# Performance work log

Measured on AMD Instinct MI355X. Metric: run time of the kernel, lower is better.

## Reference

```python
import jax, jax.numpy as jnp
import numpy as np

B, S, D, H = 4, 2048, 1024, 16
DK = D // H


def _rope(x):
    # x: [B, H, S, DK]; lucidrains rotary_embedding_torch default:
    # theta=10000, interleaved (rotate_half on (d/2, 2) pairs), freqs repeated pairwise.
    s, d = x.shape[-2], x.shape[-1]
    inv_freq = 1.0 / (10000.0 ** (jnp.arange(0, d, 2, dtype=jnp.float32) / d))  # [d/2]
    angles = jnp.arange(s, dtype=jnp.float32)[:, None] * inv_freq[None, :]      # [S, d/2]
    ang = jnp.repeat(angles, 2, axis=-1)                                        # [S, d] interleaved
    cos, sin = jnp.cos(ang), jnp.sin(ang)
    xp = x.reshape(*x.shape[:-1], d // 2, 2)
    rot = jnp.stack((-xp[..., 1], xp[..., 0]), axis=-1).reshape(x.shape)        # rotate_half
    return x * cos + rot * sin


def setup_inputs() -> dict:
    key = jax.random.key(0)
    ks = jax.random.split(key, 8)
    scale = 1.0 / np.sqrt(D)
    return {
        "q": jax.random.normal(ks[0], (B, S, D), dtype=jnp.float32),
        "k": jax.random.normal(ks[1], (B, S, D), dtype=jnp.float32),
        "v": jax.random.normal(ks[2], (B, S, D), dtype=jnp.float32),
        "mask": jax.random.randint(ks[3], (B, S), 0, 2, dtype=jnp.int32),
        "w_q": jax.random.normal(ks[4], (D, D), dtype=jnp.float32) * scale,
        "w_k": jax.random.normal(ks[5], (D, D), dtype=jnp.float32) * scale,
        "w_v": jax.random.normal(ks[6], (D, D), dtype=jnp.float32) * scale,
        "w_o": jax.random.normal(ks[7], (D, D), dtype=jnp.float32) * scale,
    }


def reference(q, k, v, mask, w_q, w_k, w_v, w_o):
    # Linear weights stored [out, in] as in torch; y = x @ W^T (bias=False).
    def split_heads(x):
        b, s, _ = x.shape
        return x.reshape(b, s, H, DK).transpose(0, 2, 1, 3)  # [B,H,S,DK]

    query = split_heads(q @ w_q.T)
    key_ = split_heads(k @ w_k.T)
    value = split_heads(v @ w_v.T)

    query = _rope(query)
    key_ = _rope(key_)

    scores = jnp.einsum("bhqd,bhkd->bhqk", query, key_) / np.sqrt(DK)
    scores = jnp.where(mask[:, None, None, :] == 0, -10000.0, scores)
    attn = jax.nn.softmax(scores, axis=-1)  # dropout is identity at eval
    x = jnp.einsum("bhqk,bhkd->bhqd", attn, value)
    x = x.transpose(0, 2, 1, 3).reshape(q.shape[0], -1, H * DK)
    return x @ w_o.T
```

## Files before the change

kernel.cpp:

```cpp
#include <hip/hip_runtime.h>
#include <hip/hip_bf16.h>
#include <math.h>


namespace {

constexpr int Bb = 4, Ss = 2048, Dd = 1024, Hh = 16, DKk = 64;

typedef __bf16 bf16;
typedef __attribute__((ext_vector_type(8))) __bf16 bf16x8;
typedef __attribute__((ext_vector_type(4))) float f32x4;

__device__ __forceinline__ bf16x8 pack8(float4 a, float4 b) {
  bf16x8 r;
  r[0] = (__bf16)a.x; r[1] = (__bf16)a.y; r[2] = (__bf16)a.z; r[3] = (__bf16)a.w;
  r[4] = (__bf16)b.x; r[5] = (__bf16)b.y; r[6] = (__bf16)b.z; r[7] = (__bf16)b.w;
  return r;
}

__device__ __forceinline__ void gl_lds16(const bf16* g, bf16* l) {
  __builtin_amdgcn_global_load_lds((const __attribute__((address_space(1))) void*)g,
                                   (__attribute__((address_space(3))) void*)l, 16, 0, 0);
}

__global__ __launch_bounds__(256) void cvt_pair(const float* __restrict__ x, bf16* __restrict__ xd,
                                                const float* __restrict__ ws, bf16* __restrict__ wd) {
  const int bid = blockIdx.x;
  const float* s; bf16* d; size_t idx;
  if (bid < 4096) { s = x; d = xd; idx = (size_t)bid * 256 + threadIdx.x; }
  else { s = ws; d = wd; idx = (size_t)(bid - 4096) * 256 + threadIdx.x; }
  idx *= 8;
  float4 f0 = *(const float4*)(s + idx), f1 = *(const float4*)(s + idx + 4);
  *(bf16x8*)(d + idx) = pack8(f0, f1);
}

__global__ __launch_bounds__(256) void cvt_w(const float* __restrict__ ws, bf16* __restrict__ wd) {
  size_t idx = ((size_t)blockIdx.x * 256 + threadIdx.x) * 8;
  float4 f0 = *(const float4*)(ws + idx), f1 = *(const float4*)(ws + idx + 4);
  *(bf16x8*)(wd + idx) = pack8(f0, f1);
}

template <int MODE>
__global__ __launch_bounds__(256) void mha_gemm(const bf16* __restrict__ A,
                                                const bf16* __restrict__ W,
                                                void* __restrict__ dstv) {
  __shared__ __align__(16) bf16 As[2][128][32];
  __shared__ __align__(16) bf16 Bs[2][128][32];
  const int tid = threadIdx.x;
  const int bm0 = blockIdx.x * 128, bn0 = blockIdx.y * 128;
  const int w = tid >> 6, lane = tid & 63, l16 = lane & 15, quad = lane >> 4;
  const int wm = (w >> 1) * 64, wn = (w & 1) * 64;
  const int lr = lane >> 2, lc = (lane & 3) * 8;

  const bf16* Ag = A + (size_t)(bm0 + w * 32 + lr) * Dd + lc;
  const bf16* Wg = W + (size_t)(bn0 + w * 32 + lr) * Dd + lc;

  f32x4 acc[4][4] = {};

  gl_lds16(Ag, &As[0][w * 32][0]);
  gl_lds16(Ag + 16 * Dd, &As[0][w * 32 + 16][0]);
  gl_lds16(Wg, &Bs[0][w * 32][0]);
  gl_lds16(Wg + 16 * Dd, &Bs[0][w * 32 + 16][0]);
  __syncthreads();

  for (int kt = 0; kt < 32; ++kt) {
    const int cur = kt & 1, nxt = cur ^ 1;
    if (kt < 31) {
      const int ko = (kt + 1) * 32;
      gl_lds16(Ag + ko, &As[nxt][w * 32][0]);
      gl_lds16(Ag + ko + 16 * Dd, &As[nxt][w * 32 + 16][0]);
      gl_lds16(Wg + ko, &Bs[nxt][w * 32][0]);
      gl_lds16(Wg + ko + 16 * Dd, &Bs[nxt][w * 32 + 16][0]);
    }
    bf16x8 af[4], bw[4];
#pragma unroll
    for (int i = 0; i < 4; ++i) af[i] = *(bf16x8*)&As[cur][wm + i * 16 + l16][quad * 8];
#pragma unroll
    for (int i = 0; i < 4; ++i) bw[i] = *(bf16x8*)&Bs[cur][wn + i * 16 + l16][quad * 8];
#pragma unroll
    for (int mt = 0; mt < 4; ++mt)
#pragma unroll
      for (int nt = 0; nt < 4; ++nt)
        acc[mt][nt] =
            __builtin_amdgcn_mfma_f32_16x16x32_bf16(af[mt], bw[nt], acc[mt][nt], 0, 0, 0);
    __syncthreads();
  }

  if constexpr (MODE == 2) {
    float* out = (float*)dstv;
#pragma unroll
    for (int mt = 0; mt < 4; ++mt)
#pragma unroll
      for (int nt = 0; nt < 4; ++nt) {
        const int gcol = bn0 + wn + nt * 16 + l16;
        const int grow0 = bm0 + wm + mt * 16 + quad * 4;
#pragma unroll
        for (int r = 0; r < 4; ++r) out[(size_t)(grow0 + r) * Dd + gcol] = acc[mt][nt][r];
      }
  } else if constexpr (MODE == 1) {
    bf16* vt = (bf16*)dstv;
#pragma unroll
    for (int mt = 0; mt < 4; ++mt)
#pragma unroll
      for (int nt = 0; nt < 4; ++nt) {
        const int gcol = bn0 + wn + nt * 16 + l16;
        const int h = gcol >> 6, dk = gcol & 63;
#pragma unroll
        for (int r = 0; r < 4; ++r) {
          const int grow = bm0 + wm + mt * 16 + quad * 4 + r;
          const int b = grow >> 11, s = grow & (Ss - 1);
          vt[((size_t)(b * Hh + h) * DKk + dk) * Ss + s] = (bf16)acc[mt][nt][r];
        }
      }
  } else {
    bf16* qp = (bf16*)dstv;
#pragma unroll
    for (int mt = 0; mt < 4; ++mt)
#pragma unroll
      for (int nt = 0; nt < 4; ++nt) {
        const int gcol = bn0 + wn + nt * 16 + l16;
        const int h = gcol >> 6, dk = gcol & 63;
        const float invf = exp2f((float)(dk >> 1) * -0.4152410118609203f);
        const float sgn = (dk & 1) ? 1.0f : -1.0f;
#pragma unroll
        for (int r = 0; r < 4; ++r) {
          const int grow = bm0 + wm + mt * 16 + quad * 4 + r;
          const int b = grow >> 11, s = grow & (Ss - 1);
          const float v = acc[mt][nt][r];
          const float ov = __shfl_xor(v, 1);
          float sn, cs;
          __sincosf((float)s * invf, &sn, &cs);
          const float rot = v * cs + sgn * ov * sn;
          qp[((size_t)(b * Hh + h) * Ss + s) * DKk + dk] = (bf16)rot;
        }
      }
  }
}

__global__ __launch_bounds__(256, 4) void mha_attn(const bf16* __restrict__ Qp,
                                                   const bf16* __restrict__ Kp,
                                                   const bf16* __restrict__ Vt,
                                                   const int* __restrict__ maskG,
                                                   bf16* __restrict__ Xo) {
  __shared__ __align__(16) bf16 Ks[2][64][64];
  __shared__ __align__(16) bf16 Vs[2][64][64];
  __shared__ __align__(16) bf16 Pbuf[4][1024];

  constexpr float c1 = 0.18033688011112042f;
  constexpr float c2 = -17.312340490667562f;

  const int tid = threadIdx.x;
  const int bh = blockIdx.y, b = bh >> 4, h = bh & 15;
  const int q0 = blockIdx.x * 128;
  const int w = tid >> 6, lane = tid & 63, l16 = lane & 15, quad = lane >> 4;
  const int swz = l16 & 7;
  const size_t hbase = (size_t)bh * Ss * DKk;

  {
    bf16* Qst = &Ks[0][0][0];
    const int row = tid >> 1, hf = tid & 1;
    const bf16* src = Qp + hbase + (size_t)(q0 + row) * DKk + hf * 32;
#pragma unroll
    for (int cc = 0; cc < 4; ++cc)
      *(int4*)&Qst[(((hf * 4 + cc) * 128) + row) * 8] = *(const int4*)(src + cc * 8);
  }
  __syncthreads();
  bf16x8 qf[2][2];
  {
    const bf16* Qst = &Ks[0][0][0];
#pragma unroll
    for (int mt = 0; mt < 2; ++mt)
#pragma unroll
      for (int kk = 0; kk < 2; ++kk)
        qf[mt][kk] = *(bf16x8*)&Qst[(((kk * 4 + quad) * 128) + w * 32 + mt * 16 + l16) * 8];
  }
  __syncthreads();

  const int srow = lane >> 3, schunk = (lane & 7) ^ (srow & 7);
  const bf16* Kg = Kp + hbase + (size_t)(w * 16 + srow) * DKk + schunk * 8;
  const bf16* Vg = Vt + ((size_t)bh * DKk + w * 16 + srow) * Ss + schunk * 8;
  const int* Mg = maskG + b * Ss + l16;

  int mcur[4], mnext[4];
#pragma unroll
  for (int i = 0; i < 2; ++i) {
    gl_lds16(Kg + (size_t)i * 8 * DKk, &Ks[0][w * 16 + i * 8][0]);
    gl_lds16(Vg + i * 8 * Ss, &Vs[0][w * 16 + i * 8][0]);
  }
#pragma unroll
  for (int nt = 0; nt < 4; ++nt) mcur[nt] = Mg[nt * 16];
  __syncthreads();

  f32x4 o[2][4] = {};
  f32x4 lo[2] = {};
  bf16* Pb = &Pbuf[w][0];

  bf16x8 vones;
#pragma unroll
  for (int i = 0; i < 8; ++i) vones[i] = (__bf16)1.0f;

  for (int kt = 0; kt < 32; ++kt) {
    const int cur = kt & 1, nxt = cur ^ 1;
    if (kt < 31) {
      const size_t k0n = (size_t)(kt + 1) * 64;
#pragma unroll
      for (int i = 0; i < 2; ++i) {
        gl_lds16(Kg + k0n * DKk + (size_t)i * 8 * DKk, &Ks[nxt][w * 16 + i * 8][0]);
        gl_lds16(Vg + k0n + i * 8 * Ss, &Vs[nxt][w * 16 + i * 8][0]);
      }
#pragma unroll
      for (int nt = 0; nt < 4; ++nt) mnext[nt] = Mg[k0n + nt * 16];
    }

    f32x4 sc[2][4];
#pragma unroll
    for (int nt = 0; nt < 4; ++nt) {
      const float bv = (mcur[nt] != 0) ? 0.0f : -1e9f;
#pragma unroll
      for (int r = 0; r < 4; ++r) { sc[0][nt][r] = bv; sc[1][nt][r] = bv; }
    }
#pragma unroll
    for (int kk = 0; kk < 2; ++kk)
#pragma unroll
      for (int nt = 0; nt < 4; ++nt) {
        bf16x8 kf = *(bf16x8*)&Ks[cur][nt * 16 + l16][((kk * 4 + quad) ^ swz) * 8];
        sc[0][nt] = __builtin_amdgcn_mfma_f32_16x16x32_bf16(qf[0][kk], kf, sc[0][nt], 0, 0, 0);
        sc[1][nt] = __builtin_amdgcn_mfma_f32_16x16x32_bf16(qf[1][kk], kf, sc[1][nt], 0, 0, 0);
      }

    bf16x8 pf0[2], pf1[2];
#pragma unroll
    for (int nt = 0; nt < 4; ++nt) {
      const int c = nt * 2 + (l16 >> 3);
      const int jj = l16 & 7;
#pragma unroll
      for (int r = 0; r < 4; ++r)
        Pb[(c * 16 + quad * 4 + r) * 8 + jj] = (bf16)exp2f(fmaf(sc[0][nt][r], c1, c2));
    }
#pragma unroll
    for (int kk = 0; kk < 2; ++kk)
      pf0[kk] = *(bf16x8*)(Pb + ((kk * 4 + quad) * 16 + l16) * 8);
#pragma unroll
    for (int nt = 0; nt < 4; ++nt) {
      const int c = nt * 2 + (l16 >> 3);
      const int jj = l16 & 7;
#pragma unroll
      for (int r = 0; r < 4; ++r)
        Pb[(c * 16 + quad * 4 + r) * 8 + jj] = (bf16)exp2f(fmaf(sc[1][nt][r], c1, c2));
    }
#pragma unroll
    for (int kk = 0; kk < 2; ++kk)
      pf1[kk] = *(bf16x8*)(Pb + ((kk * 4 + quad) * 16 + l16) * 8);

#pragma unroll
    for (int kk = 0; kk < 2; ++kk) {
      lo[0] = __builtin_amdgcn_mfma_f32_16x16x32_bf16(pf0[kk], vones, lo[0], 0, 0, 0);
      lo[1] = __builtin_amdgcn_mfma_f32_16x16x32_bf16(pf1[kk], vones, lo[1], 0, 0, 0);
#pragma unroll
      for (int nt = 0; nt < 4; ++nt) {
        bf16x8 vf = *(bf16x8*)&Vs[cur][nt * 16 + l16][((kk * 4 + quad) ^ swz) * 8];
        o[0][nt] = __builtin_amdgcn_mfma_f32_16x16x32_bf16(pf0[kk], vf, o[0][nt], 0, 0, 0);
        o[1][nt] = __builtin_amdgcn_mfma_f32_16x16x32_bf16(pf1[kk], vf, o[1][nt], 0, 0, 0);
      }
    }
    __syncthreads();
#pragma unroll
    for (int nt = 0; nt < 4; ++nt) mcur[nt] = mnext[nt];
  }

#pragma unroll
  for (int mt = 0; mt < 2; ++mt)
#pragma unroll
    for (int nt = 0; nt < 4; ++nt)
#pragma unroll
      for (int r = 0; r < 4; ++r) {
        const int srw = q0 + w * 32 + mt * 16 + quad * 4 + r;
        const int dk = nt * 16 + l16;
        Xo[(size_t)(b * Ss + srw) * Dd + h * DKk + dk] = (bf16)(o[mt][nt][r] / lo[mt][r]);
      }
}

}

extern "C" void kernel_launch(void* const* d_in, const int* in_sizes, int n_in,
                              void* d_out, int out_size, void* d_ws, size_t ws_size,
                              hipStream_t stream) {
  (void)in_sizes; (void)n_in; (void)out_size; (void)ws_size;
  const float* q = (const float*)d_in[0];
  const float* k = (const float*)d_in[1];
  const float* v = (const float*)d_in[2];
  const int* mask = (const int*)d_in[3];
  const float* w_q = (const float*)d_in[4];
  const float* w_k = (const float*)d_in[5];
  const float* w_v = (const float*)d_in[6];
  const float* w_o = (const float*)d_in[7];
  float* out = (float*)d_out;

  const size_t n_elem = (size_t)Bb * Hh * Ss * DKk;
  bf16* buf0 = (bf16*)d_ws;
  bf16* wbuf = buf0 + n_elem;
  bf16* Qp = wbuf + (1 << 20);
  bf16* Kp = Qp + n_elem;
  bf16* Vt = Kp + n_elem;

  dim3 g(64, 8), blk(256);
  cvt_pair<<<4608, blk, 0, stream>>>(q, buf0, w_q, wbuf);
  mha_gemm<0><<<g, blk, 0, stream>>>(buf0, wbuf, (void*)Qp);
  cvt_pair<<<4608, blk, 0, stream>>>(k, buf0, w_k, wbuf);
  mha_gemm<0><<<g, blk, 0, stream>>>(buf0, wbuf, (void*)Kp);
  cvt_pair<<<4608, blk, 0, stream>>>(v, buf0, w_v, wbuf);
  mha_gemm<1><<<g, blk, 0, stream>>>(buf0, wbuf, (void*)Vt);
  mha_attn<<<dim3(16, 64), blk, 0, stream>>>(Qp, Kp, Vt, mask, buf0);
  cvt_w<<<512, blk, 0, stream>>>(w_o, wbuf);
  mha_gemm<2><<<g, blk, 0, stream>>>(buf0, wbuf, (void*)out);
}
```

Before: 400.0 us.

## Double GEMM K-tile to 64 with XOR-swizzled LDS layout and occupancy hint

Increases the projection GEMM K-tile from 32 to 64, halving the number of main-loop iterations and barriers. Stores A and W tiles in LDS with an XOR swizzle on 16-byte chunks, applied to the global source addresses since global_load_lds writes contiguously, to avoid bank conflicts on the fragment reads. Adds a launch bound of 2 blocks per SM. LDS use doubles to 64KB per block, which may limit occupancy.

```diff
diff --git a/kernel.cpp b/kernel.cpp
--- a/kernel.cpp
+++ b/kernel.cpp
@@ -41,48 +41,56 @@
 }
 
 template <int MODE>
-__global__ __launch_bounds__(256) void mha_gemm(const bf16* __restrict__ A,
-                                                const bf16* __restrict__ W,
-                                                void* __restrict__ dstv) {
-  __shared__ __align__(16) bf16 As[2][128][32];
-  __shared__ __align__(16) bf16 Bs[2][128][32];
+__global__ __launch_bounds__(256, 2) void mha_gemm(const bf16* __restrict__ A,
+                                                   const bf16* __restrict__ W,
+                                                   void* __restrict__ dstv) {
+  __shared__ __align__(16) bf16 As[2][128][64];
+  __shared__ __align__(16) bf16 Bs[2][128][64];
   const int tid = threadIdx.x;
   const int bm0 = blockIdx.x * 128, bn0 = blockIdx.y * 128;
   const int w = tid >> 6, lane = tid & 63, l16 = lane & 15, quad = lane >> 4;
   const int wm = (w >> 1) * 64, wn = (w & 1) * 64;
-  const int lr = lane >> 2, lc = (lane & 3) * 8;
-
-  const bf16* Ag = A + (size_t)(bm0 + w * 32 + lr) * Dd + lc;
-  const bf16* Wg = W + (size_t)(bn0 + w * 32 + lr) * Dd + lc;
+  const int swz = l16 & 7;
+
+  const int srow = lane >> 3, schunk = (lane & 7) ^ (srow & 7);
+  const bf16* Ag = A + (size_t)(bm0 + w * 32 + srow) * Dd + schunk * 8;
+  const bf16* Wg = W + (size_t)(bn0 + w * 32 + srow) * Dd + schunk * 8;
 
   f32x4 acc[4][4] = {};
 
-  gl_lds16(Ag, &As[0][w * 32][0]);
-  gl_lds16(Ag + 16 * Dd, &As[0][w * 32 + 16][0]);
-  gl_lds16(Wg, &Bs[0][w * 32][0]);
-  gl_lds16(Wg + 16 * Dd, &Bs[0][w * 32 + 16][0]);
+#pragma unroll
+  for (int i = 0; i < 4; ++i) {
+    gl_lds16(Ag + (size_t)i * 8 * Dd, &As[0][w * 32 + i * 8][0]);
+    gl_lds16(Wg + (size_t)i * 8 * Dd, &Bs[0][w * 32 + i * 8][0]);
+  }
   __syncthreads();
 
-  for (int kt = 0; kt < 32; ++kt) {
+  for (int kt = 0; kt < 16; ++kt) {
     const int cur = kt & 1, nxt = cur ^ 1;
-    if (kt < 31) {
-      const int ko = (kt + 1) * 32;
-      gl_lds16(Ag + ko, &As[nxt][w * 32][0]);
-      gl_lds16(Ag + ko + 16 * Dd, &As[nxt][w * 32 + 16][0]);
-      gl_lds16(Wg + ko, &Bs[nxt][w * 32][0]);
-      gl_lds16(Wg + ko + 16 * Dd, &Bs[nxt][w * 32 + 16][0]);
-    }
-    bf16x8 af[4], bw[4];
-#pragma unroll
-    for (int i = 0; i < 4; ++i) af[i] = *(bf16x8*)&As[cur][wm + i * 16 + l16][quad * 8];
-#pragma unroll
-    for (int i = 0; i < 4; ++i) bw[i] = *(bf16x8*)&Bs[cur][wn + i * 16 + l16][quad * 8];
-#pragma unroll
-    for (int mt = 0; mt < 4; ++mt)
-#pragma unroll
-      for (int nt = 0; nt < 4; ++nt)
-        acc[mt][nt] =
-            __builtin_amdgcn_mfma_f32_16x16x32_bf16(af[mt], bw[nt], acc[mt][nt], 0, 0, 0);
+    if (kt < 15) {
+      const int ko = (kt + 1) * 64;
+#pragma unroll
+      for (int i = 0; i < 4; ++i) {
+        gl_lds16(Ag + ko + (size_t)i * 8 * Dd, &As[nxt][w * 32 + i * 8][0]);
+        gl_lds16(Wg + ko + (size_t)i * 8 * Dd, &Bs[nxt][w * 32 + i * 8][0]);
+      }
+    }
+#pragma unroll
+    for (int kk = 0; kk < 2; ++kk) {
+      bf16x8 af[4], bw[4];
+#pragma unroll
+      for (int i = 0; i < 4; ++i)
+        af[i] = *(bf16x8*)&As[cur][wm + i * 16 + l16][((kk * 4 + quad) ^ swz) * 8];
+#pragma unroll
+      for (int i = 0; i < 4; ++i)
+        bw[i] = *(bf16x8*)&Bs[cur][wn + i * 16 + l16][((kk * 4 + quad) ^ swz) * 8];
+#pragma unroll
+      for (int mt = 0; mt < 4; ++mt)
+#pragma unroll
+        for (int nt = 0; nt < 4; ++nt)
+          acc[mt][nt] =
+              __builtin_amdgcn_mfma_f32_16x16x32_bf16(af[mt], bw[nt], acc[mt][nt], 0, 0, 0);
+    }
     __syncthreads();
   }
 
```

Result: faster. 390.8 us (-2.3%).
